# Performance work log

Hardware: AMD Instinct MI355X
Metric: run time of the kernel (lower is better)

## Reference

```python
import jax, jax.numpy as jnp
import numpy as np

B, T, D = 128, 32, 1024
ADA, INTER, RANK = 1024, 1024, 8
LN_EPS = 1e-5

def setup_inputs() -> dict:
    key = jax.random.key(0)
    ks = jax.random.split(key, 9)
    return {
        "x": jax.random.normal(ks[0], (B, T, D), dtype=jnp.float32),
        "ada_emb": jax.random.normal(ks[1], (B, ADA), dtype=jnp.float32),
        "base_layer": jax.random.normal(ks[2], (D, D), dtype=jnp.float32),  # torch.randn init
        "w1": jax.random.normal(ks[3], (ADA, INTER), dtype=jnp.float32) * 0.02,
        "b1": jnp.zeros((INTER,), dtype=jnp.float32),
        "w2": jax.random.normal(ks[4], (INTER, 2 * D * RANK), dtype=jnp.float32) * 0.02,
        "b2": jnp.zeros((2 * D * RANK,), dtype=jnp.float32),
        "ln_g": jnp.ones((ADA,), dtype=jnp.float32),
        "ln_b": jnp.zeros((ADA,), dtype=jnp.float32),
    }

def _layernorm(x, g, b):
    mu = jnp.mean(x, axis=-1, keepdims=True)
    var = jnp.var(x, axis=-1, keepdims=True)
    return (x - mu) * jax.lax.rsqrt(var + LN_EPS) * g + b

def reference(x, ada_emb, base_layer, w1, b1, w2, b2, ln_g, ln_b):
    b, t, d = x.shape
    # hypernetwork: cond -> per-sample LoRA factors
    ae = _layernorm(ada_emb, ln_g, ln_b)
    h = jax.nn.gelu(ae @ w1 + b1, approximate=False)  # nn.GELU is exact (erf)
    xw = h @ w2 + b2                                   # (B, 2*D*rank)
    x_a, x_b = jnp.split(xw, 2, axis=-1)
    x_a = x_a.reshape(b, d, RANK)
    x_b = x_b.reshape(b, d, RANK)
    # fused per-sample weight: base + x_a @ x_b^T  -> (B, D, D)
    layer = base_layer[None, :, :] + jnp.einsum('bdr,bkr->bdk', x_a, x_b)
    # apply shared per-sample weight to every token (equiv to repeat_interleave + bmm)
    out = jnp.einsum('btc,bco->bto', x, layer)
    return x + out  # residual=True
```

## Files before the change

kernel.cpp:

```cpp
#include <hip/hip_runtime.h>
#include <hip/hip_bf16.h>
#include <math.h>

#define BB    128
#define TT    32
#define DD    1024
#define NADA  1024
#define NINT  1024
#define NRANK 8
#define LNEPS 1e-5f
#define TKCH  8

using bf16x8 = __attribute__((ext_vector_type(8))) short;
using f32x4  = __attribute__((ext_vector_type(4))) float;

__device__ __forceinline__ short f2bf(float f) {
    __hip_bfloat16 h = __float2bfloat16(f);
    return *reinterpret_cast<short*>(&h);
}

__device__ __forceinline__ void async16(const void* g, void* l) {
    __builtin_amdgcn_global_load_lds(
        (const __attribute__((address_space(1))) void*)g,
        (__attribute__((address_space(3))) void*)l, 16, 0, 0);
}

__device__ __forceinline__ void tcast_tile(
    const float* __restrict__ in, short* __restrict__ out, int K, int N,
    int bx, int by, bool addI, int tid, float (*t)[68])
{
    const int n0 = bx * 64, k0 = by * 64;
    #pragma unroll
    for (int it = 0; it < 4; ++it) {
        const int idx = it * 256 + tid;
        const int r = idx >> 4, c4 = (idx & 15) * 4;
        float4 v = *(const float4*)(in + (size_t)(k0 + r) * N + n0 + c4);
        t[r][c4 + 0] = v.x; t[r][c4 + 1] = v.y;
        t[r][c4 + 2] = v.z; t[r][c4 + 3] = v.w;
    }
    __syncthreads();
    #pragma unroll
    for (int it = 0; it < 4; ++it) {
        const int idx = it * 256 + tid;
        const int rn = idx >> 4, c4 = (idx & 15) * 4;
        float f0 = t[c4 + 0][rn], f1 = t[c4 + 1][rn];
        float f2 = t[c4 + 2][rn], f3 = t[c4 + 3][rn];
        if (addI) {
            const int n = n0 + rn;
            if (k0 + c4 + 0 == n) f0 += 1.f;
            if (k0 + c4 + 1 == n) f1 += 1.f;
            if (k0 + c4 + 2 == n) f2 += 1.f;
            if (k0 + c4 + 3 == n) f3 += 1.f;
        }
        short4 p;
        p.x = f2bf(f0); p.y = f2bf(f1); p.z = f2bf(f2); p.w = f2bf(f3);
        *(short4*)(out + (size_t)(n0 + rn) * K + k0 + c4) = p;
    }
}

__global__ __launch_bounds__(256) void prep_kernel(
    const float* __restrict__ x, const float* __restrict__ w1,
    const float* __restrict__ base, const float* __restrict__ w2,
    const float* __restrict__ ada, const float* __restrict__ lng,
    const float* __restrict__ lnb,
    short* __restrict__ x_bf, short* __restrict__ w1t,
    short* __restrict__ baset, short* __restrict__ w2t,
    short* __restrict__ ae_bf)
{
    __shared__ float t[64][68];
    const int bid = blockIdx.x, tid = threadIdx.x;

    if (bid < 4096) {
        tcast_tile(w2, w2t, NINT, 2 * DD * NRANK, bid & 255, bid >> 8, false, tid, t);
    } else if (bid < 6144) {
        const int b = bid - 4096;
        const int i0 = b * 512 + tid;
        float4 v0 = reinterpret_cast<const float4*>(x)[i0];
        float4 v1 = reinterpret_cast<const float4*>(x)[i0 + 256];
        short4 p0, p1;
        p0.x = f2bf(v0.x); p0.y = f2bf(v0.y); p0.z = f2bf(v0.z); p0.w = f2bf(v0.w);
        p1.x = f2bf(v1.x); p1.y = f2bf(v1.y); p1.z = f2bf(v1.z); p1.w = f2bf(v1.w);
        reinterpret_cast<short4*>(x_bf)[i0] = p0;
        reinterpret_cast<short4*>(x_bf)[i0 + 256] = p1;
    } else if (bid < 6400) {
        const int b = bid - 6144;
        tcast_tile(w1, w1t, NADA, NINT, b & 15, b >> 4, false, tid, t);
    } else if (bid < 6656) {
        const int b = bid - 6400;
        tcast_tile(base, baset, DD, DD, b & 15, b >> 4, true, tid, t);
    } else {
        const int b = bid - 6656;
        const float* row = ada + (size_t)b * NADA;
        float sum = 0.f, sumsq = 0.f;
        for (int i = tid; i < NADA; i += 256) {
            float v = row[i];
            sum += v; sumsq += v * v;
        }
        #pragma unroll
        for (int off = 32; off > 0; off >>= 1) {
            sum   += __shfl_down(sum, off);
            sumsq += __shfl_down(sumsq, off);
        }
        float* s1 = &t[0][0];
        float* s2 = &t[1][0];
        const int wid = tid >> 6, lane = tid & 63;
        if (lane == 0) { s1[wid] = sum; s2[wid] = sumsq; }
        __syncthreads();
        if (tid == 0) {
            float a = 0.f, c = 0.f;
            for (int i = 0; i < 4; ++i) { a += s1[i]; c += s2[i]; }
            s1[0] = a; s2[0] = c;
        }
        __syncthreads();
        const float mu  = s1[0] * (1.f / NADA);
        const float var = s2[0] * (1.f / NADA) - mu * mu;
        const float inv = rsqrtf(var + LNEPS);
        for (int i = tid; i < NADA; i += 256) {
            ae_bf[(size_t)b * NADA + i] = f2bf((row[i] - mu) * inv * lng[i] + lnb[i]);
        }
    }
}

template <int BM, int BN, int WM, int WN, int EPI>
__global__ __launch_bounds__(256, 2) void mgemm(
    const short* __restrict__ A, const short* __restrict__ Bt,
    const float* __restrict__ bias, float* __restrict__ C,
    int M, int N, int K, int kLen,
    const float* __restrict__ tp, const float* __restrict__ xw)
{
    constexpr int MT = BM / WM / 16;
    constexpr int NT = BN / WN / 16;
    constexpr int LA = BM / 64;
    constexpr int LB = BN / 64;

    __shared__ __align__(16) short As[BM * 32];
    __shared__ __align__(16) short Bs[BN * 32];
    __shared__ float tmS[(EPI == 2) ? BM * 8 : 1];
    __shared__ float xbS[(EPI == 2) ? (BM / 32) * BN * 8 : 1];

    const int bm = blockIdx.y * BM;
    const int bn = blockIdx.x * BN;
    const int tid = threadIdx.x;
    const int wave = tid >> 6, lane = tid & 63;
    const int wm0 = (wave / WN) * (BM / WM);
    const int wn0 = (wave % WN) * (BN / WN);
    const int quad = lane >> 4, r16 = lane & 15;

    if constexpr (EPI == 2) {
        float4 a = {0.f, 0.f, 0.f, 0.f};
        #pragma unroll
        for (int ch = 0; ch < TKCH; ++ch) {
            float4 v = *(const float4*)(tp + (size_t)ch * BB * TT * NRANK
                                           + (size_t)bm * 8 + tid * 4);
            a.x += v.x; a.y += v.y; a.z += v.z; a.w += v.w;
        }
        *(float4*)&tmS[tid * 4] = a;
        const int b0 = bm >> 5;
        const int grp = tid >> 6;
        const int inner = tid & 63;
        const float* src = xw + (size_t)(b0 + grp) * (2 * DD * NRANK) + DD * NRANK
                              + (size_t)bn * 8;
        *(float4*)&xbS[grp * BN * 8 + inner * 8]     = *(const float4*)(src + inner * 8);
        *(float4*)&xbS[grp * BN * 8 + inner * 8 + 4] = *(const float4*)(src + inner * 8 + 4);
    }

    f32x4 acc[MT][NT] = {};

    for (int k0 = 0; k0 < kLen; k0 += 32) {
        #pragma unroll
        for (int s = 0; s < LA; ++s) {
            const int c = s * 256 + tid;
            async16(A + (size_t)(bm + (c >> 2)) * K + k0 + (c & 3) * 8, &As[c * 8]);
        }
        #pragma unroll
        for (int s = 0; s < LB; ++s) {
            const int c = s * 256 + tid;
            async16(Bt + (size_t)(bn + (c >> 2)) * K + k0 + (c & 3) * 8, &Bs[c * 8]);
        }
        __syncthreads();
        bf16x8 af[MT], bfr[NT];
        #pragma unroll
        for (int i = 0; i < MT; ++i)
            af[i] = *reinterpret_cast<const bf16x8*>(&As[(wm0 + i * 16 + r16) * 32 + quad * 8]);
        #pragma unroll
        for (int j = 0; j < NT; ++j)
            bfr[j] = *reinterpret_cast<const bf16x8*>(&Bs[(wn0 + j * 16 + r16) * 32 + quad * 8]);
        #pragma unroll
        for (int i = 0; i < MT; ++i)
            #pragma unroll
            for (int j = 0; j < NT; ++j)
                acc[i][j] = __builtin_amdgcn_mfma_f32_16x16x32_bf16(
                    af[i], bfr[j], acc[i][j], 0, 0, 0);
        __syncthreads();
    }

    if constexpr (EPI == 2) {
        float xbr[NT][8];
        #pragma unroll
        for (int i = 0; i < MT; ++i) {
            const int mlBase = wm0 + i * 16 + quad * 4;
            const int s = mlBase >> 5;
            #pragma unroll
            for (int j = 0; j < NT; ++j) {
                const int nl = wn0 + j * 16 + r16;
                #pragma unroll
                for (int rr = 0; rr < 8; ++rr)
                    xbr[j][rr] = xbS[(s * BN + nl) * 8 + rr];
            }
            #pragma unroll
            for (int r = 0; r < 4; ++r) {
                const int ml = mlBase + r;
                const int m = bm + ml;
                float t8[8];
                #pragma unroll
                for (int rr = 0; rr < 8; ++rr) t8[rr] = tmS[ml * 8 + rr];
                #pragma unroll
                for (int j = 0; j < NT; ++j) {
                    const int n = bn + wn0 + j * 16 + r16;
                    float v = acc[i][j][r];
                    #pragma unroll
                    for (int rr = 0; rr < 8; ++rr) v += t8[rr] * xbr[j][rr];
                    C[(size_t)m * N + n] = v;
                }
            }
        }
    } else {
        #pragma unroll
        for (int i = 0; i < MT; ++i) {
            #pragma unroll
            for (int r = 0; r < 4; ++r) {
                const int m = bm + wm0 + i * 16 + quad * 4 + r;
                #pragma unroll
                for (int j = 0; j < NT; ++j) {
                    const int n = bn + wn0 + j * 16 + r16;
                    float v = acc[i][j][r] + bias[n];
                    if (EPI == 1) {
                        C[(size_t)m * N + n] = v;
                    } else {
                        v = 0.5f * v * (1.f + erff(v * 0.70710678118654752f));
                        ((short*)C)[(size_t)m * N + n] = f2bf(v);
                    }
                }
            }
        }
    }
}

__global__ __launch_bounds__(256) void tpart_kernel(
    const float* __restrict__ x, const float* __restrict__ xw,
    float* __restrict__ tp)
{
    __shared__ float xa[(DD / TKCH) * NRANK];
    const int b = blockIdx.x, ch = blockIdx.y;
    const float* src = xw + (size_t)b * (2 * DD * NRANK) + (size_t)ch * (DD / TKCH) * NRANK;
    float4 v = *(const float4*)(src + threadIdx.x * 4);
    *(float4*)(xa + threadIdx.x * 4) = v;
    __syncthreads();
    const int m = threadIdx.x >> 3;
    const int r = threadIdx.x & 7;
    const float* xrow = x + ((size_t)b * TT + m) * DD + ch * (DD / TKCH);
    float accv = 0.f;
    #pragma unroll 4
    for (int c = 0; c < DD / TKCH; c += 4) {
        float4 xr = *(const float4*)(xrow + c);
        accv += xr.x * xa[(c + 0) * NRANK + r];
        accv += xr.y * xa[(c + 1) * NRANK + r];
        accv += xr.z * xa[(c + 2) * NRANK + r];
        accv += xr.w * xa[(c + 3) * NRANK + r];
    }
    tp[((size_t)ch * BB * TT + (size_t)b * TT + m) * NRANK + r] = accv;
}

extern "C" void kernel_launch(void* const* d_in, const int* in_sizes, int n_in,
                              void* d_out, int out_size, void* d_ws, size_t ws_size,
                              hipStream_t stream)
{
    const float* x    = (const float*)d_in[0];
    const float* ada  = (const float*)d_in[1];
    const float* base = (const float*)d_in[2];
    const float* w1   = (const float*)d_in[3];
    const float* b1   = (const float*)d_in[4];
    const float* w2   = (const float*)d_in[5];
    const float* b2   = (const float*)d_in[6];
    const float* lng  = (const float*)d_in[7];
    const float* lnb  = (const float*)d_in[8];
    float* out = (float*)d_out;

    char* w = (char*)d_ws;
    short* x_bf  = (short*)w;  w += (size_t)8 << 20;
    short* w2t   = (short*)w;  w += (size_t)32 << 20;
    short* w1t   = (short*)w;  w += (size_t)2 << 20;
    short* baset = (short*)w;  w += (size_t)2 << 20;
    short* ae_bf = (short*)w;  w += (size_t)256 << 10;
    short* h_bf  = (short*)w;  w += (size_t)256 << 10;
    float* xw    = (float*)w;  w += (size_t)8 << 20;
    float* tp    = (float*)w;

    prep_kernel<<<6784, 256, 0, stream>>>(
        x, w1, base, w2, ada, lng, lnb, x_bf, w1t, baset, w2t, ae_bf);
    mgemm<64, 64, 2, 2, 3><<<dim3(NINT / 64, BB / 64), 256, 0, stream>>>(
        ae_bf, w1t, b1, (float*)h_bf, BB, NINT, NADA, NADA, nullptr, nullptr);
    mgemm<64, 64, 2, 2, 1><<<dim3(2 * DD * NRANK / 64, BB / 64), 256, 0, stream>>>(
        h_bf, w2t, b2, xw, BB, 2 * DD * NRANK, NINT, NINT, nullptr, nullptr);
    tpart_kernel<<<dim3(BB, TKCH), 256, 0, stream>>>(x, xw, tp);
    mgemm<128, 64, 2, 2, 2><<<dim3(DD / 64, BB * TT / 128), 256, 0, stream>>>(
        x_bf, baset, nullptr, out, BB * TT, DD, DD, DD, tp, xw);
}
```

Before: 196.4 us.

## Read fp32 w2 directly in GEMM, drop transpose-cast, split-K both hypernet GEMMs

Removes the prep pass that transposed and cast the 64MB fp32 w2 to bf16. A new GEMM reads fp32 w2 straight into LDS and converts it to bf16 on the fly, with split-K of 2 and atomicAdd into an xw buffer pre-seeded with b2. The first hypernet GEMM now uses split-K of 4 followed by a separate combine kernel that adds the bias and applies GELU. The intent is to avoid a full extra read and write of w2 and to raise parallelism for M=128. The cost is fp32 atomics, an extra launch, and strided per-element LDS conversion in the inner loop.

```diff
diff --git a/kernel.cpp b/kernel.cpp
--- a/kernel.cpp
+++ b/kernel.cpp
@@ -10,6 +10,7 @@
 #define NRANK 8
 #define LNEPS 1e-5f
 #define TKCH  8
+#define SPL2  4
 
 using bf16x8 = __attribute__((ext_vector_type(8))) short;
 using f32x4  = __attribute__((ext_vector_type(4))) float;
@@ -60,21 +61,18 @@
 
 __global__ __launch_bounds__(256) void prep_kernel(
     const float* __restrict__ x, const float* __restrict__ w1,
-    const float* __restrict__ base, const float* __restrict__ w2,
-    const float* __restrict__ ada, const float* __restrict__ lng,
-    const float* __restrict__ lnb,
+    const float* __restrict__ base, const float* __restrict__ ada,
+    const float* __restrict__ lng, const float* __restrict__ lnb,
+    const float* __restrict__ b2,
     short* __restrict__ x_bf, short* __restrict__ w1t,
-    short* __restrict__ baset, short* __restrict__ w2t,
-    short* __restrict__ ae_bf)
+    short* __restrict__ baset, short* __restrict__ ae_bf,
+    float* __restrict__ xw)
 {
     __shared__ float t[64][68];
     const int bid = blockIdx.x, tid = threadIdx.x;
 
-    if (bid < 4096) {
-        tcast_tile(w2, w2t, NINT, 2 * DD * NRANK, bid & 255, bid >> 8, false, tid, t);
-    } else if (bid < 6144) {
-        const int b = bid - 4096;
-        const int i0 = b * 512 + tid;
+    if (bid < 2048) {
+        const int i0 = bid * 512 + tid;
         float4 v0 = reinterpret_cast<const float4*>(x)[i0];
         float4 v1 = reinterpret_cast<const float4*>(x)[i0 + 256];
         short4 p0, p1;
@@ -82,14 +80,14 @@
         p1.x = f2bf(v1.x); p1.y = f2bf(v1.y); p1.z = f2bf(v1.z); p1.w = f2bf(v1.w);
         reinterpret_cast<short4*>(x_bf)[i0] = p0;
         reinterpret_cast<short4*>(x_bf)[i0 + 256] = p1;
-    } else if (bid < 6400) {
-        const int b = bid - 6144;
+    } else if (bid < 2304) {
+        const int b = bid - 2048;
         tcast_tile(w1, w1t, NADA, NINT, b & 15, b >> 4, false, tid, t);
-    } else if (bid < 6656) {
-        const int b = bid - 6400;
+    } else if (bid < 2560) {
+        const int b = bid - 2304;
         tcast_tile(base, baset, DD, DD, b & 15, b >> 4, true, tid, t);
-    } else {
-        const int b = bid - 6656;
+    } else if (bid < 2688) {
+        const int b = bid - 2560;
         const float* row = ada + (size_t)b * NADA;
         float sum = 0.f, sumsq = 0.f;
         for (int i = tid; i < NADA; i += 256) {
@@ -118,14 +116,17 @@
         for (int i = tid; i < NADA; i += 256) {
             ae_bf[(size_t)b * NADA + i] = f2bf((row[i] - mu) * inv * lng[i] + lnb[i]);
         }
+    } else {
+        const int i0 = (bid - 2688) * 1024 + tid * 4;
+        const int n0 = i0 & (2 * DD * NRANK - 1);
+        *(float4*)(xw + i0) = *(const float4*)(b2 + n0);
     }
 }
 
 template <int BM, int BN, int WM, int WN, int EPI>
 __global__ __launch_bounds__(256, 2) void mgemm(
     const short* __restrict__ A, const short* __restrict__ Bt,
-    const float* __restrict__ bias, float* __restrict__ C,
-    int M, int N, int K, int kLen,
+    float* __restrict__ C, int M, int N, int K, int kLen,
     const float* __restrict__ tp, const float* __restrict__ xw)
 {
     constexpr int MT = BM / WM / 16;
@@ -140,6 +141,7 @@
 
     const int bm = blockIdx.y * BM;
     const int bn = blockIdx.x * BN;
+    const int kStart = blockIdx.z * kLen;
     const int tid = threadIdx.x;
     const int wave = tid >> 6, lane = tid & 63;
     const int wm0 = (wave / WN) * (BM / WM);
@@ -166,7 +168,8 @@
 
     f32x4 acc[MT][NT] = {};
 
-    for (int k0 = 0; k0 < kLen; k0 += 32) {
+    for (int kt = 0; kt < kLen; kt += 32) {
+        const int k0 = kStart + kt;
         #pragma unroll
         for (int s = 0; s < LA; ++s) {
             const int c = s * 256 + tid;
@@ -233,17 +236,93 @@
                 #pragma unroll
                 for (int j = 0; j < NT; ++j) {
                     const int n = bn + wn0 + j * 16 + r16;
-                    float v = acc[i][j][r] + bias[n];
-                    if (EPI == 1) {
-                        C[(size_t)m * N + n] = v;
-                    } else {
-                        v = 0.5f * v * (1.f + erff(v * 0.70710678118654752f));
-                        ((short*)C)[(size_t)m * N + n] = f2bf(v);
-                    }
+                    C[((size_t)blockIdx.z * M + m) * N + n] = acc[i][j][r];
                 }
             }
         }
     }
+}
+
+template <int SPLITK>
+__global__ __launch_bounds__(256, 2) void gemm_w2(
+    const short* __restrict__ A, const float* __restrict__ W,
+    float* __restrict__ C, int M, int N, int K)
+{
+    constexpr int BM = 128, BN = 64;
+    constexpr int MT = 4, NT = 2;
+    __shared__ __align__(16) short As[BM * 32];
+    __shared__ __align__(16) float Bf[32 * BN];
+
+    const int bn = blockIdx.x * BN;
+    const int kLen = K / SPLITK;
+    const int kStart = blockIdx.z * kLen;
+    const int tid = threadIdx.x;
+    const int wave = tid >> 6, lane = tid & 63;
+    const int wm0 = (wave >> 1) * 64;
+    const int wn0 = (wave & 1) * 32;
+    const int quad = lane >> 4, r16 = lane & 15;
+
+    f32x4 acc[MT][NT] = {};
+
+    for (int kt = 0; kt < kLen; kt += 32) {
+        const int k0 = kStart + kt;
+        #pragma unroll
+        for (int s = 0; s < 2; ++s) {
+            const int c = s * 256 + tid;
+            async16(A + (size_t)(c >> 2) * K + k0 + (c & 3) * 8, &As[c * 8]);
+        }
+        #pragma unroll
+        for (int s = 0; s < 2; ++s) {
+            const int c = s * 256 + tid;
+            async16(W + (size_t)(k0 + (c >> 4)) * N + bn + (c & 15) * 4, &Bf[c * 4]);
+        }
+        __syncthreads();
+        bf16x8 af[MT], bfr[NT];
+        #pragma unroll
+        for (int i = 0; i < MT; ++i)
+            af[i] = *reinterpret_cast<const bf16x8*>(&As[(wm0 + i * 16 + r16) * 32 + quad * 8]);
+        #pragma unroll
+        for (int j = 0; j < NT; ++j) {
+            const int n = wn0 + j * 16 + r16;
+            short tmp[8];
+            #pragma unroll
+            for (int t = 0; t < 8; ++t)
+                tmp[t] = f2bf(Bf[(quad * 8 + t) * BN + n]);
+            bfr[j] = *reinterpret_cast<const bf16x8*>(tmp);
+        }
+        #pragma unroll
+        for (int i = 0; i < MT; ++i)
+            #pragma unroll
+            for (int j = 0; j < NT; ++j)
+                acc[i][j] = __builtin_amdgcn_mfma_f32_16x16x32_bf16(
+                    af[i], bfr[j], acc[i][j], 0, 0, 0);
+        __syncthreads();
+    }
+
+    #pragma unroll
+    for (int i = 0; i < MT; ++i) {
+        #pragma unroll
+        for (int r = 0; r < 4; ++r) {
+            const int m = wm0 + i * 16 + quad * 4 + r;
+            #pragma unroll
+            for (int j = 0; j < NT; ++j) {
+                const int n = bn + wn0 + j * 16 + r16;
+                atomicAdd(&C[(size_t)m * N + n], acc[i][j][r]);
+            }
+        }
+    }
+}
+
+__global__ __launch_bounds__(256) void combine_gelu(
+    const float* __restrict__ part, const float* __restrict__ b1,
+    short* __restrict__ h)
+{
+    const int idx = blockIdx.x * 256 + threadIdx.x;
+    float s = b1[idx & (NINT - 1)];
+    #pragma unroll
+    for (int z = 0; z < SPL2; ++z) s += part[(size_t)z * BB * NINT + idx];
+    s = 0.5f * s * (1.f + erff(s * 0.70710678118654752f));
+    h[idx] = f2bf(s);
 }
 
 __global__ __launch_bounds__(256) void tpart_kernel(
@@ -288,21 +367,22 @@
 
     char* w = (char*)d_ws;
     short* x_bf  = (short*)w;  w += (size_t)8 << 20;
-    short* w2t   = (short*)w;  w += (size_t)32 << 20;
     short* w1t   = (short*)w;  w += (size_t)2 << 20;
     short* baset = (short*)w;  w += (size_t)2 << 20;
     short* ae_bf = (short*)w;  w += (size_t)256 << 10;
     short* h_bf  = (short*)w;  w += (size_t)256 << 10;
     float* xw    = (float*)w;  w += (size_t)8 << 20;
-    float* tp    = (float*)w;
-
-    prep_kernel<<<6784, 256, 0, stream>>>(
-        x, w1, base, w2, ada, lng, lnb, x_bf, w1t, baset, w2t, ae_bf);
-    mgemm<64, 64, 2, 2, 3><<<dim3(NINT / 64, BB / 64), 256, 0, stream>>>(
-        ae_bf, w1t, b1, (float*)h_bf, BB, NINT, NADA, NADA, nullptr, nullptr);
-    mgemm<64, 64, 2, 2, 1><<<dim3(2 * DD * NRANK / 64, BB / 64), 256, 0, stream>>>(
-        h_bf, w2t, b2, xw, BB, 2 * DD * NRANK, NINT, NINT, nullptr, nullptr);
+    float* tp    = (float*)w;  w += (size_t)1 << 20;
+    float* part  = (float*)w;
+
+    prep_kernel<<<4736, 256, 0, stream>>>(
+        x, w1, base, ada, lng, lnb, b2, x_bf, w1t, baset, ae_bf, xw);
+    mgemm<64, 64, 2, 2, 0><<<dim3(NINT / 64, BB / 64, SPL2), 256, 0, stream>>>(
+        ae_bf, w1t, part, BB, NINT, NADA, NADA / SPL2, nullptr, nullptr);
+    combine_gelu<<<BB * NINT / 256, 256, 0, stream>>>(part, b1, h_bf);
+    gemm_w2<2><<<dim3(2 * DD * NRANK / 64, 1, 2), 256, 0, stream>>>(
+        h_bf, w2, xw, BB, 2 * DD * NRANK, NINT);
     tpart_kernel<<<dim3(BB, TKCH), 256, 0, stream>>>(x, xw, tp);
     mgemm<128, 64, 2, 2, 2><<<dim3(DD / 64, BB * TT / 128), 256, 0, stream>>>(
-        x_bf, baset, nullptr, out, BB * TT, DD, DD, DD, tp, xw);
-}
+        x_bf, baset, out, BB * TT, DD, DD, DD, tp, xw);
+}
```

Result: faster. 189.6 us (-3.5%).
